# Performance work log

Measured on AMD Instinct MI355X. Metric: run time of the kernel, lower is better.

## Reference

```python
import jax, jax.numpy as jnp
import numpy as np

B, S, D, H = 4, 1024, 1024, 16
DH = D // H  # 64
SCALE = 1.0 / np.sqrt(D)  # module uses 1/sqrt(d_model), not d_head


def _mh(t):
    # [B,S,D] -> [B*H,S,DH]
    b, s, _ = t.shape
    return t.reshape(b, s, H, DH).transpose(0, 2, 1, 3).reshape(b * H, s, DH)


def _shift(t):
    # pad one zero at FRONT of last dim, reinterpret (row-major) as [BH,L+1,S], drop first row
    bh, s, l = t.shape
    t = jnp.concatenate([jnp.zeros((bh, s, 1), t.dtype), t], axis=-1)
    return t.reshape(bh, l + 1, s)[:, 1:, :]


def setup_inputs() -> dict:
    key = jax.random.key(0)
    ks = jax.random.split(key, 12)
    w_sc = 1.0 / np.sqrt(D)
    return {
        "x": jax.random.normal(ks[0], (B, S, D), jnp.float32),
        "u": jax.random.normal(ks[1], (DH,), jnp.float32) * 0.02,
        "v": jax.random.normal(ks[2], (DH,), jnp.float32) * 0.02,
        "pos": jax.random.normal(ks[3], (B, S, D), jnp.float32),
        "Wq": jax.random.normal(ks[4], (D, D), jnp.float32) * w_sc,
        "bq": jnp.zeros((D,), jnp.float32),
        "Wk": jax.random.normal(ks[5], (D, D), jnp.float32) * w_sc,
        "bk": jnp.zeros((D,), jnp.float32),
        "Wv": jax.random.normal(ks[6], (D, D), jnp.float32) * w_sc,
        "bv": jnp.zeros((D,), jnp.float32),
        "Wc": jax.random.normal(ks[7], (D, D), jnp.float32) * w_sc,
        "bc": jnp.zeros((D,), jnp.float32),
    }


def reference(x, u, v, pos, Wq, bq, Wk, bk, Wv, bv, Wc, bc):
    q = _mh(x @ Wq.T + bq)      # [BH,S,DH]
    k = _mh(x @ Wk.T + bk)      # [BH,S,DH]
    w = _mh(x @ Wv.T + bv)      # [BH,S,DH]
    r = _mh(pos)                # [BH,S,DH]
    ac = jnp.einsum('bjk,bmk->bjm', q + u, k)          # content-content  [BH,S,S]
    bd = _shift(jnp.einsum('bjk,blk->bjl', q + v, r))  # content-position [BH,S,S]
    att = jax.nn.softmax((ac + bd) * SCALE, axis=-1)   # dropout is identity (eval)
    o = att @ w                                        # [BH,S,DH]
    o = o.reshape(B, H, S, DH).transpose(0, 2, 1, 3).reshape(B, S, D)
    return o @ Wc.T + bc
```

## Files before the change

kernel.cpp:

```cpp
#include <hip/hip_runtime.h>
#include <hip/hip_bf16.h>


typedef __bf16 bf16x8 __attribute__((ext_vector_type(8)));
typedef float  f32x4  __attribute__((ext_vector_type(4)));
typedef unsigned short u16x4 __attribute__((ext_vector_type(4)));

struct alignas(16) U128 { unsigned long long lo, hi; };

__device__ __forceinline__ bf16x8 ldg8(const __hip_bfloat16* p) {
    U128 u = *reinterpret_cast<const U128*>(p);
    return __builtin_bit_cast(bf16x8, u);
}

__device__ __forceinline__ __bf16 f2b(float f) {
    __hip_bfloat16 h = __float2bfloat16(f);
    return __builtin_bit_cast(__bf16, h);
}
__device__ __forceinline__ unsigned short f2bu(float f) {
    __hip_bfloat16 h = __float2bfloat16(f);
    return __builtin_bit_cast(unsigned short, h);
}
__device__ __forceinline__ float b2f(__bf16 b) {
    __hip_bfloat16 h = __builtin_bit_cast(__hip_bfloat16, b);
    return __bfloat162float(h);
}
__device__ __forceinline__ float bu2f(unsigned short u) {
    __hip_bfloat16 h = __builtin_bit_cast(__hip_bfloat16, u);
    return __bfloat162float(h);
}

__device__ __forceinline__ bf16x8 ldg8cvt(const float* p) {
    f32x4 a = *reinterpret_cast<const f32x4*>(p);
    f32x4 b = *reinterpret_cast<const f32x4*>(p + 4);
    bf16x8 r;
    r[0] = f2b(a[0]); r[1] = f2b(a[1]); r[2] = f2b(a[2]); r[3] = f2b(a[3]);
    r[4] = f2b(b[0]); r[5] = f2b(b[1]); r[6] = f2b(b[2]); r[7] = f2b(b[3]);
    return r;
}

#define MFMA16(a, b, c) __builtin_amdgcn_mfma_f32_16x16x32_bf16((a), (b), (c), 0, 0, 0)

__device__ __forceinline__ void gll16(const __hip_bfloat16* g, void* lds_wave_base) {
    __builtin_amdgcn_global_load_lds(
        (const __attribute__((address_space(1))) void*)g,
        (__attribute__((address_space(3))) void*)lds_wave_base,
        16, 0, 0);
}

__global__ __launch_bounds__(256) void cvt_kernel(
    const float* __restrict__ x,  const float* __restrict__ pos,
    const float* __restrict__ wq, const float* __restrict__ wk,
    const float* __restrict__ wv, const float* __restrict__ wc,
    __hip_bfloat16* __restrict__ xb, __hip_bfloat16* __restrict__ posb,
    __hip_bfloat16* __restrict__ wqkvb, __hip_bfloat16* __restrict__ wcb)
{
    const size_t base = ((size_t)blockIdx.x * 256 + threadIdx.x) * 8;
    const size_t M1 = (size_t)1 << 20;
    const float* src; __hip_bfloat16* dst; size_t o;
    if (base < 4*M1)        { src = x;   dst = xb;           o = base; }
    else if (base < 8*M1)   { src = pos; dst = posb;         o = base - 4*M1; }
    else if (base < 9*M1)   { src = wq;  dst = wqkvb;        o = base - 8*M1; }
    else if (base < 10*M1)  { src = wk;  dst = wqkvb + M1;   o = base - 9*M1; }
    else if (base < 11*M1)  { src = wv;  dst = wqkvb + 2*M1; o = base - 10*M1; }
    else                    { src = wc;  dst = wcb;          o = base - 11*M1; }
    *(bf16x8*)(dst + o) = ldg8cvt(src + o);
}

__global__ __launch_bounds__(256) void gemm_qkv(
    const __hip_bfloat16* __restrict__ A,
    const __hip_bfloat16* __restrict__ Bm,
    const float* __restrict__ bq, const float* __restrict__ bk,
    const float* __restrict__ bv, const float* __restrict__ u,
    __hip_bfloat16* __restrict__ Qu,
    __hip_bfloat16* __restrict__ Kb, __hip_bfloat16* __restrict__ Vt)
{
    __shared__ __hip_bfloat16 As[128 * 32];
    __shared__ __hip_bfloat16 Bs[128 * 32];

    const int tid  = threadIdx.x;
    const int lane = tid & 63, w = tid >> 6;
    const int quad = lane >> 4, c16 = lane & 15;
    const int wm = w >> 1, wn = w & 1;
    const int m0 = blockIdx.y * 128;
    const int n0 = blockIdx.x * 128;

    const int srow = w * 16 + (lane >> 2);
    const int scol = (lane & 3) * 8;
    const __hip_bfloat16* gA0 = A  + (size_t)(m0 + srow) * 1024 + scol;
    const __hip_bfloat16* gA1 = gA0 + (size_t)64 * 1024;
    const __hip_bfloat16* gB0 = Bm + (size_t)(n0 + srow) * 1024 + scol;
    const __hip_bfloat16* gB1 = gB0 + (size_t)64 * 1024;
    char* ldsA0 = (char*)As + (w << 10);
    char* ldsA1 = ldsA0 + 4096;
    char* ldsB0 = (char*)Bs + (w << 10);
    char* ldsB1 = ldsB0 + 4096;

    f32x4 acc[4][4] = {};

    for (int k0 = 0; k0 < 1024; k0 += 32) {
        gll16(gA0 + k0, ldsA0);
        gll16(gA1 + k0, ldsA1);
        gll16(gB0 + k0, ldsB0);
        gll16(gB1 + k0, ldsB1);
        __syncthreads();

        bf16x8 af[4], bfr[4];
        #pragma unroll
        for (int i = 0; i < 4; ++i) {
            af[i]  = *(const bf16x8*)&As[(wm * 64 + i * 16 + c16) * 32 + quad * 8];
            bfr[i] = *(const bf16x8*)&Bs[(wn * 64 + i * 16 + c16) * 32 + quad * 8];
        }
        #pragma unroll
        for (int mi = 0; mi < 4; ++mi)
            #pragma unroll
            for (int ni = 0; ni < 4; ++ni)
                acc[mi][ni] = MFMA16(af[mi], bfr[ni], acc[mi][ni]);
        __syncthreads();
    }

    #pragma unroll
    for (int mi = 0; mi < 4; ++mi) {
        #pragma unroll
        for (int ni = 0; ni < 4; ++ni) {
            const int m = m0 + wm * 64 + mi * 16 + quad * 4;
            const int n = n0 + wn * 64 + ni * 16 + c16;
            if (n < 1024) {
                const float b0 = bq[n] + u[n & 63];
                #pragma unroll
                for (int r = 0; r < 4; ++r)
                    Qu[(size_t)(m + r) * 1024 + n] =
                        __float2bfloat16(acc[mi][ni][r] + b0);
            } else if (n < 2048) {
                const int nn = n - 1024;
                const float b0 = bk[nn];
                #pragma unroll
                for (int r = 0; r < 4; ++r)
                    Kb[(size_t)(m + r) * 1024 + nn] =
                        __float2bfloat16(acc[mi][ni][r] + b0);
            } else {
                const int nn = n - 2048;
                const float b0 = bv[nn];
                const int d = nn & 63, hh = nn >> 6;
                const int bb = m >> 10, s = m & 1023;
                u16x4 pk;
                #pragma unroll
                for (int r = 0; r < 4; ++r)
                    pk[r] = f2bu(acc[mi][ni][r] + b0);
                *(u16x4*)&Vt[(((size_t)(bb * 16 + hh) * 64 + d) << 10) + s] = pk;
            }
        }
    }
}

__global__ __launch_bounds__(256) void gemm_fin64(
    const __hip_bfloat16* __restrict__ A,
    const __hip_bfloat16* __restrict__ Bm,
    float* __restrict__ dout, const float* __restrict__ bc)
{
    __shared__ __hip_bfloat16 As[64 * 32];
    __shared__ __hip_bfloat16 Bs[64 * 32];

    const int tid  = threadIdx.x;
    const int lane = tid & 63, w = tid >> 6;
    const int quad = lane >> 4, c16 = lane & 15;
    const int wm = w >> 1, wn = w & 1;
    const int m0 = blockIdx.y * 64;
    const int n0 = blockIdx.x * 64;

    const int srow = w * 16 + (lane >> 2);
    const int scol = (lane & 3) * 8;
    const __hip_bfloat16* gA = A  + (size_t)(m0 + srow) * 1024 + scol;
    const __hip_bfloat16* gB = Bm + (size_t)(n0 + srow) * 1024 + scol;
    char* ldsA = (char*)As + (w << 10);
    char* ldsB = (char*)Bs + (w << 10);

    f32x4 acc[2][2] = {};

    for (int k0 = 0; k0 < 1024; k0 += 32) {
        gll16(gA + k0, ldsA);
        gll16(gB + k0, ldsB);
        __syncthreads();

        bf16x8 af[2], bfr[2];
        #pragma unroll
        for (int i = 0; i < 2; ++i) {
            af[i]  = *(const bf16x8*)&As[(wm * 32 + i * 16 + c16) * 32 + quad * 8];
            bfr[i] = *(const bf16x8*)&Bs[(wn * 32 + i * 16 + c16) * 32 + quad * 8];
        }
        #pragma unroll
        for (int mi = 0; mi < 2; ++mi)
            #pragma unroll
            for (int ni = 0; ni < 2; ++ni)
                acc[mi][ni] = MFMA16(af[mi], bfr[ni], acc[mi][ni]);
        __syncthreads();
    }

    #pragma unroll
    for (int mi = 0; mi < 2; ++mi) {
        #pragma unroll
        for (int ni = 0; ni < 2; ++ni) {
            const int m = m0 + wm * 32 + mi * 16 + quad * 4;
            const int n = n0 + wn * 32 + ni * 16 + c16;
            const float b0 = bc[n];
            #pragma unroll
            for (int r = 0; r < 4; ++r)
                dout[(size_t)(m + r) * 1024 + n] = acc[mi][ni][r] + b0;
        }
    }
}

__device__ __forceinline__ int lidx16(int row, int c) {
    return (row << 10) + ((((c >> 3) ^ row) << 3) | (c & 7));
}

__global__ __launch_bounds__(512, 4) void attn_kernel(
    const __hip_bfloat16* __restrict__ Qu,
    const __hip_bfloat16* __restrict__ Kb,
    const __hip_bfloat16* __restrict__ Posb,
    const __hip_bfloat16* __restrict__ Vt,
    const float* __restrict__ uvec, const float* __restrict__ vvec,
    __hip_bfloat16* __restrict__ O)
{
    __shared__ __attribute__((aligned(16))) __hip_bfloat16 Ls[32 * 1024];
    __shared__ float q2s[64];
    __shared__ float Wsum[32 * 8];
    __shared__ float rs[32];

    const int tid  = threadIdx.x;
    const int lane = tid & 63, w = tid >> 6;
    const int quad = lane >> 4, c16 = lane & 15;
    const int i0 = blockIdx.y * 32;
    const int bh = blockIdx.x;
    const int b = bh >> 4, h = bh & 15;
    const size_t headoff = (size_t)h * 64;
    const size_t tokbase = (size_t)b * 1024;
    const int j2 = i0 + 32;

    if (tid < 64) {
        float val = 0.f;
        if (j2 < 1024)
            val = b2f(__builtin_bit_cast(__bf16,
                      Qu[(tokbase + j2) * 1024 + headoff + tid])) +
                  (vvec[tid] - uvec[tid]);
        q2s[tid] = val;
    }
    __syncthreads();

    if (tid < 32) {
        const int i = i0 + tid;
        if (i + 1 < 1024) Ls[lidx16(tid, i + 1)] = __float2bfloat16(0.f);
    }

    const __hip_bfloat16* qup0 =
        Qu + (tokbase + i0 + c16) * 1024 + headoff + quad * 8;

    {
        bf16x8 a[2][2];
        #pragma unroll
        for (int g = 0; g < 2; ++g) {
            a[g][0] = ldg8(qup0 + (size_t)g * 16 * 1024);
            a[g][1] = ldg8(qup0 + (size_t)g * 16 * 1024 + 32);
            #pragma unroll
            for (int j = 0; j < 8; ++j) {
                const int d = quad * 8 + j;
                a[g][0][j] = f2b(b2f(a[g][0][j]) + (vvec[d] - uvec[d]));
                a[g][1][j] = f2b(b2f(a[g][1][j]) + (vvec[d + 32] - uvec[d + 32]));
            }
        }
        for (int t = 0; t < 8; ++t) {
            const int l0 = w * 128 + t * 16;
            const __hip_bfloat16* rp =
                Posb + (tokbase + l0 + c16) * 1024 + headoff + quad * 8;
            const bf16x8 r0 = ldg8(rp);
            const bf16x8 r1 = ldg8(rp + 32);
            const int lq = l0 + quad * 4;
            #pragma unroll
            for (int g = 0; g < 2; ++g) {
                f32x4 c = (f32x4){0.f, 0.f, 0.f, 0.f};
                c = MFMA16(r0, a[g][0], c);
                c = MFMA16(r1, a[g][1], c);
                const int jl = g * 16 + c16;
                const int base2 = lq + i0 + jl + 1;
                const int rwm1 = jl - 1;
                #pragma unroll
                for (int r = 0; r < 4; ++r) {
                    const int t1 = base2 + r;
                    const int cc = t1 & 1023;
                    const int rw = rwm1 + (t1 >> 10);
                    if (rw >= 0)
                        Ls[lidx16(rw, cc)] = __float2bfloat16(c[r]);
                }
            }
        }
    }

    if (j2 < 1024) {
        for (int c = i0 + 33 + tid; c < 1024; c += 512) {
            const int l = c - i0 - 33;
            const __hip_bfloat16* rp = Posb + (tokbase + l) * 1024 + headoff;
            float s = 0.f;
            #pragma unroll
            for (int d8 = 0; d8 < 8; ++d8) {
                const bf16x8 rv = ldg8(rp + d8 * 8);
                #pragma unroll
                for (int jj = 0; jj < 8; ++jj)
                    s += q2s[d8 * 8 + jj] * b2f(rv[jj]);
            }
            Ls[lidx16(31, c)] = __float2bfloat16(s);
        }
    }
    __syncthreads();

    {
        bf16x8 au[2][2];
        #pragma unroll
        for (int g = 0; g < 2; ++g) {
            au[g][0] = ldg8(qup0 + (size_t)g * 16 * 1024);
            au[g][1] = ldg8(qup0 + (size_t)g * 16 * 1024 + 32);
        }
        const float C1 = 1.44269504f * 0.03125f;
        const float C2 = -5.77078016f;
        float rsum[2] = {0.f, 0.f};
        for (int t = 0; t < 8; ++t) {
            const int c0 = w * 128 + t * 16;
            const __hip_bfloat16* kp =
                Kb + (tokbase + c0 + c16) * 1024 + headoff + quad * 8;
            const bf16x8 k0 = ldg8(kp);
            const bf16x8 k1 = ldg8(kp + 32);
            const int cc0 = c0 + quad * 4;
            #pragma unroll
            for (int g = 0; g < 2; ++g) {
                f32x4 c = (f32x4){0.f, 0.f, 0.f, 0.f};
                c = MFMA16(k0, au[g][0], c);
                c = MFMA16(k1, au[g][1], c);
                const int jl = g * 16 + c16;
                const int idx = lidx16(jl, cc0);
                const u16x4 bd = *(const u16x4*)&Ls[idx];
                u16x4 pk;
                float s4 = 0.f;
                #pragma unroll
                for (int r = 0; r < 4; ++r) {
                    const float lg = bu2f(bd[r]) + c[r];
                    const float p = __builtin_amdgcn_exp2f(fmaf(lg, C1, C2));
                    s4 += p;
                    pk[r] = f2bu(p);
                }
                *(u16x4*)&Ls[idx] = pk;
                s4 += __shfl_xor(s4, 16);
                s4 += __shfl_xor(s4, 32);
                rsum[g] += s4;
            }
        }
        if (lane < 16) {
            Wsum[lane * 8 + w] = rsum[0];
            Wsum[(16 + lane) * 8 + w] = rsum[1];
        }
    }
    __syncthreads();

    if (tid < 32) {
        float s = 0.f;
        #pragma unroll
        for (int k = 0; k < 8; ++k) s += Wsum[tid * 8 + k];
        rs[tid] = 1.f / s;
    }
    __syncthreads();

    {
        const int d0 = (w & 3) * 16;
        const int kh = w >> 2;
        const __hip_bfloat16* vp =
            Vt + ((size_t)bh * 64 + d0 + c16) * 1024 + quad * 8;
        f32x4 acc[2] = {};
        for (int kk = kh * 512; kk < kh * 512 + 512; kk += 32) {
            const bf16x8 vld = ldg8(vp + kk);
            #pragma unroll
            for (int g = 0; g < 2; ++g) {
                const bf16x8 p =
                    *(const bf16x8*)&Ls[lidx16(g * 16 + c16, kk + quad * 8)];
                acc[g] = MFMA16(p, vld, acc[g]);
            }
        }
        __syncthreads();
        float* Lf = (float*)Ls;
        const int sbase = (w & 3) * 1024;
        if (kh == 1) {
            #pragma unroll
            for (int g = 0; g < 2; ++g)
                #pragma unroll
                for (int r = 0; r < 4; ++r)
                    Lf[sbase + g * 256 + (quad * 4 + r) * 16 + c16] = acc[g][r];
        }
        __syncthreads();
        if (kh == 0) {
            #pragma unroll
            for (int g = 0; g < 2; ++g)
                #pragma unroll
                for (int r = 0; r < 4; ++r) {
                    const int il = g * 16 + quad * 4 + r;
                    const float val =
                        (acc[g][r] + Lf[sbase + g * 256 + (quad * 4 + r) * 16 + c16])
                        * rs[il];
                    const int i = i0 + il;
                    const int d = d0 + c16;
                    O[(tokbase + i) * 1024 + headoff + d] = __float2bfloat16(val);
                }
        }
    }
}

extern "C" void kernel_launch(void* const* d_in, const int* in_sizes, int n_in,
                              void* d_out, int out_size, void* d_ws, size_t ws_size,
                              hipStream_t stream)
{
    const float* x   = (const float*)d_in[0];
    const float* u   = (const float*)d_in[1];
    const float* v   = (const float*)d_in[2];
    const float* pos = (const float*)d_in[3];
    const float* Wq  = (const float*)d_in[4];
    const float* bq  = (const float*)d_in[5];
    const float* Wk  = (const float*)d_in[6];
    const float* bk  = (const float*)d_in[7];
    const float* Wv  = (const float*)d_in[8];
    const float* bv  = (const float*)d_in[9];
    const float* Wc  = (const float*)d_in[10];
    const float* bc  = (const float*)d_in[11];

    const size_t MB = (size_t)1 << 20;
    char* ws = (char*)d_ws;
    __hip_bfloat16* Qu    = (__hip_bfloat16*)(ws + 0 * MB);
    __hip_bfloat16* Kb    = (__hip_bfloat16*)(ws + 8 * MB);
    __hip_bfloat16* Vt    = (__hip_bfloat16*)(ws + 16 * MB);
    __hip_bfloat16* xb    = (__hip_bfloat16*)(ws + 24 * MB);
    __hip_bfloat16* O     = (__hip_bfloat16*)(ws + 24 * MB);
    __hip_bfloat16* Posb  = (__hip_bfloat16*)(ws + 32 * MB);
    __hip_bfloat16* Wqkvb = (__hip_bfloat16*)(ws + 40 * MB);
    __hip_bfloat16* Wcb   = (__hip_bfloat16*)(ws + 46 * MB);

    cvt_kernel<<<6144, 256, 0, stream>>>(x, pos, Wq, Wk, Wv, Wc,
                                         xb, Posb, Wqkvb, Wcb);

    gemm_qkv<<<dim3(24, 32), dim3(256), 0, stream>>>(
        xb, Wqkvb, bq, bk, bv, u, Qu, Kb, Vt);

    attn_kernel<<<dim3(64, 32), dim3(512), 0, stream>>>(
        Qu, Kb, Posb, Vt, u, v, O);

    gemm_fin64<<<dim3(16, 64), dim3(256), 0, stream>>>(
        O, Wcb, (float*)d_out, bc);
}
```

Before: 289.6 us.

## Double attention row tile to 64 and enlarge output GEMM tiles to 128x128

```diff
diff --git a/kernel.cpp b/kernel.cpp
--- a/kernel.cpp
+++ b/kernel.cpp
@@ -153,55 +153,61 @@
     }
 }
 
-__global__ __launch_bounds__(256) void gemm_fin64(
+__global__ __launch_bounds__(256) void gemm_fin(
     const __hip_bfloat16* __restrict__ A,
     const __hip_bfloat16* __restrict__ Bm,
     float* __restrict__ dout, const float* __restrict__ bc)
 {
-    __shared__ __hip_bfloat16 As[64 * 32];
-    __shared__ __hip_bfloat16 Bs[64 * 32];
+    __shared__ __hip_bfloat16 As[128 * 32];
+    __shared__ __hip_bfloat16 Bs[128 * 32];
 
     const int tid  = threadIdx.x;
     const int lane = tid & 63, w = tid >> 6;
     const int quad = lane >> 4, c16 = lane & 15;
     const int wm = w >> 1, wn = w & 1;
-    const int m0 = blockIdx.y * 64;
-    const int n0 = blockIdx.x * 64;
+    const int m0 = blockIdx.y * 128;
+    const int n0 = blockIdx.x * 128;
 
     const int srow = w * 16 + (lane >> 2);
     const int scol = (lane & 3) * 8;
-    const __hip_bfloat16* gA = A  + (size_t)(m0 + srow) * 1024 + scol;
-    const __hip_bfloat16* gB = Bm + (size_t)(n0 + srow) * 1024 + scol;
-    char* ldsA = (char*)As + (w << 10);
-    char* ldsB = (char*)Bs + (w << 10);
-
-    f32x4 acc[2][2] = {};
+    const __hip_bfloat16* gA0 = A  + (size_t)(m0 + srow) * 1024 + scol;
+    const __hip_bfloat16* gA1 = gA0 + (size_t)64 * 1024;
+    const __hip_bfloat16* gB0 = Bm + (size_t)(n0 + srow) * 1024 + scol;
+    const __hip_bfloat16* gB1 = gB0 + (size_t)64 * 1024;
+    char* ldsA0 = (char*)As + (w << 10);
+    char* ldsA1 = ldsA0 + 4096;
+    char* ldsB0 = (char*)Bs + (w << 10);
+    char* ldsB1 = ldsB0 + 4096;
+
+    f32x4 acc[4][4] = {};
 
     for (int k0 = 0; k0 < 1024; k0 += 32) {
-        gll16(gA + k0, ldsA);
-        gll16(gB + k0, ldsB);
-        __syncthreads();
-
-        bf16x8 af[2], bfr[2];
-        #pragma unroll
-        for (int i = 0; i < 2; ++i) {
-            af[i]  = *(const bf16x8*)&As[(wm * 32 + i * 16 + c16) * 32 + quad * 8];
-            bfr[i] = *(const bf16x8*)&Bs[(wn * 32 + i * 16 + c16) * 32 + quad * 8];
-        }
-        #pragma unroll
-        for (int mi = 0; mi < 2; ++mi)
-            #pragma unroll
-            for (int ni = 0; ni < 2; ++ni)
+        gll16(gA0 + k0, ldsA0);
+        gll16(gA1 + k0, ldsA1);
+        gll16(gB0 + k0, ldsB0);
+        gll16(gB1 + k0, ldsB1);
+        __syncthreads();
+
+        bf16x8 af[4], bfr[4];
+        #pragma unroll
+        for (int i = 0; i < 4; ++i) {
+            af[i]  = *(const bf16x8*)&As[(wm * 64 + i * 16 + c16) * 32 + quad * 8];
+            bfr[i] = *(const bf16x8*)&Bs[(wn * 64 + i * 16 + c16) * 32 + quad * 8];
+        }
+        #pragma unroll
+        for (int mi = 0; mi < 4; ++mi)
+            #pragma unroll
+            for (int ni = 0; ni < 4; ++ni)
                 acc[mi][ni] = MFMA16(af[mi], bfr[ni], acc[mi][ni]);
         __syncthreads();
     }
 
     #pragma unroll
-    for (int mi = 0; mi < 2; ++mi) {
-        #pragma unroll
-        for (int ni = 0; ni < 2; ++ni) {
-            const int m = m0 + wm * 32 + mi * 16 + quad * 4;
-            const int n = n0 + wn * 32 + ni * 16 + c16;
+    for (int mi = 0; mi < 4; ++mi) {
+        #pragma unroll
+        for (int ni = 0; ni < 4; ++ni) {
+            const int m = m0 + wm * 64 + mi * 16 + quad * 4;
+            const int n = n0 + wn * 64 + ni * 16 + c16;
             const float b0 = bc[n];
             #pragma unroll
             for (int r = 0; r < 4; ++r)
@@ -214,7 +220,7 @@
     return (row << 10) + ((((c >> 3) ^ row) << 3) | (c & 7));
 }
 
-__global__ __launch_bounds__(512, 4) void attn_kernel(
+__global__ __launch_bounds__(512, 2) void attn_kernel(
     const __hip_bfloat16* __restrict__ Qu,
     const __hip_bfloat16* __restrict__ Kb,
     const __hip_bfloat16* __restrict__ Posb,
@@ -222,32 +228,22 @@
     const float* __restrict__ uvec, const float* __restrict__ vvec,
     __hip_bfloat16* __restrict__ O)
 {
-    __shared__ __attribute__((aligned(16))) __hip_bfloat16 Ls[32 * 1024];
-    __shared__ float q2s[64];
-    __shared__ float Wsum[32 * 8];
-    __shared__ float rs[32];
+    __shared__ __attribute__((aligned(16))) __hip_bfloat16 Ls[64 * 1024];
+    __shared__ float Wsum[64 * 8];
+    __shared__ float rs[64];
 
     const int tid  = threadIdx.x;
     const int lane = tid & 63, w = tid >> 6;
     const int quad = lane >> 4, c16 = lane & 15;
-    const int i0 = blockIdx.y * 32;
+    const int i0 = blockIdx.y * 64;
     const int bh = blockIdx.x;
     const int b = bh >> 4, h = bh & 15;
     const size_t headoff = (size_t)h * 64;
     const size_t tokbase = (size_t)b * 1024;
-    const int j2 = i0 + 32;
+    const int j2 = i0 + 64;
+    const bool havej2 = (j2 < 1024);
 
     if (tid < 64) {
-        float val = 0.f;
-        if (j2 < 1024)
-            val = b2f(__builtin_bit_cast(__bf16,
-                      Qu[(tokbase + j2) * 1024 + headoff + tid])) +
-                  (vvec[tid] - uvec[tid]);
-        q2s[tid] = val;
-    }
-    __syncthreads();
-
-    if (tid < 32) {
         const int i = i0 + tid;
         if (i + 1 < 1024) Ls[lidx16(tid, i + 1)] = __float2bfloat16(0.f);
     }
@@ -256,9 +252,9 @@
         Qu + (tokbase + i0 + c16) * 1024 + headoff + quad * 8;
 
     {
-        bf16x8 a[2][2];
-        #pragma unroll
-        for (int g = 0; g < 2; ++g) {
+        bf16x8 a[4][2];
+        #pragma unroll
+        for (int g = 0; g < 4; ++g) {
             a[g][0] = ldg8(qup0 + (size_t)g * 16 * 1024);
             a[g][1] = ldg8(qup0 + (size_t)g * 16 * 1024 + 32);
             #pragma unroll
@@ -266,6 +262,17 @@
                 const int d = quad * 8 + j;
                 a[g][0][j] = f2b(b2f(a[g][0][j]) + (vvec[d] - uvec[d]));
                 a[g][1][j] = f2b(b2f(a[g][1][j]) + (vvec[d + 32] - uvec[d + 32]));
+            }
+        }
+        bf16x8 a4[2];
+        if (havej2) {
+            a4[0] = ldg8(qup0 + (size_t)64 * 1024);
+            a4[1] = ldg8(qup0 + (size_t)64 * 1024 + 32);
+            #pragma unroll
+            for (int j = 0; j < 8; ++j) {
+                const int d = quad * 8 + j;
+                a4[0][j] = f2b(b2f(a4[0][j]) + (vvec[d] - uvec[d]));
+                a4[1][j] = f2b(b2f(a4[1][j]) + (vvec[d + 32] - uvec[d + 32]));
             }
         }
         for (int t = 0; t < 8; ++t) {
@@ -276,7 +283,7 @@
             const bf16x8 r1 = ldg8(rp + 32);
             const int lq = l0 + quad * 4;
             #pragma unroll
-            for (int g = 0; g < 2; ++g) {
+            for (int g = 0; g < 4; ++g) {
                 f32x4 c = (f32x4){0.f, 0.f, 0.f, 0.f};
                 c = MFMA16(r0, a[g][0], c);
                 c = MFMA16(r1, a[g][1], c);
@@ -292,36 +299,33 @@
                         Ls[lidx16(rw, cc)] = __float2bfloat16(c[r]);
                 }
             }
-        }
-    }
-
-    if (j2 < 1024) {
-        for (int c = i0 + 33 + tid; c < 1024; c += 512) {
-            const int l = c - i0 - 33;
-            const __hip_bfloat16* rp = Posb + (tokbase + l) * 1024 + headoff;
-            float s = 0.f;
-            #pragma unroll
-            for (int d8 = 0; d8 < 8; ++d8) {
-                const bf16x8 rv = ldg8(rp + d8 * 8);
-                #pragma unroll
-                for (int jj = 0; jj < 8; ++jj)
-                    s += q2s[d8 * 8 + jj] * b2f(rv[jj]);
-            }
-            Ls[lidx16(31, c)] = __float2bfloat16(s);
+            if (havej2) {
+                f32x4 c = (f32x4){0.f, 0.f, 0.f, 0.f};
+                c = MFMA16(r0, a4[0], c);
+                c = MFMA16(r1, a4[1], c);
+                if (c16 == 0) {
+                    #pragma unroll
+                    for (int r = 0; r < 4; ++r) {
+                        const int cc = lq + r + i0 + 65;
+                        if (cc < 1024)
+                            Ls[lidx16(63, cc)] = __float2bfloat16(c[r]);
+                    }
+                }
+            }
         }
     }
     __syncthreads();
 
     {
-        bf16x8 au[2][2];
-        #pragma unroll
-        for (int g = 0; g < 2; ++g) {
+        bf16x8 au[4][2];
+        #pragma unroll
+        for (int g = 0; g < 4; ++g) {
             au[g][0] = ldg8(qup0 + (size_t)g * 16 * 1024);
             au[g][1] = ldg8(qup0 + (size_t)g * 16 * 1024 + 32);
         }
         const float C1 = 1.44269504f * 0.03125f;
         const float C2 = -5.77078016f;
-        float rsum[2] = {0.f, 0.f};
+        float rsum[4] = {0.f, 0.f, 0.f, 0.f};
         for (int t = 0; t < 8; ++t) {
             const int c0 = w * 128 + t * 16;
             const __hip_bfloat16* kp =
@@ -330,7 +334,7 @@
             const bf16x8 k1 = ldg8(kp + 32);
             const int cc0 = c0 + quad * 4;
             #pragma unroll
-            for (int g = 0; g < 2; ++g) {
+            for (int g = 0; g < 4; ++g) {
                 f32x4 c = (f32x4){0.f, 0.f, 0.f, 0.f};
                 c = MFMA16(k0, au[g][0], c);
                 c = MFMA16(k1, au[g][1], c);
@@ -353,13 +357,14 @@
             }
         }
         if (lane < 16) {
-            Wsum[lane * 8 + w] = rsum[0];
-            Wsum[(16 + lane) * 8 + w] = rsum[1];
+            #pragma unroll
+            for (int g = 0; g < 4; ++g)
+                Wsum[(g * 16 + lane) * 8 + w] = rsum[g];
         }
     }
     __syncthreads();
 
-    if (tid < 32) {
+    if (tid < 64) {
         float s = 0.f;
         #pragma unroll
         for (int k = 0; k < 8; ++k) s += Wsum[tid * 8 + k];
@@ -372,11 +377,11 @@
         const int kh = w >> 2;
         const __hip_bfloat16* vp =
             Vt + ((size_t)bh * 64 + d0 + c16) * 1024 + quad * 8;
-        f32x4 acc[2] = {};
+        f32x4 acc[4] = {};
         for (int kk = kh * 512; kk < kh * 512 + 512; kk += 32) {
             const bf16x8 vld = ldg8(vp + kk);
             #pragma unroll
-            for (int g = 0; g < 2; ++g) {
+            for (int g = 0; g < 4; ++g) {
                 const bf16x8 p =
                     *(const bf16x8*)&Ls[lidx16(g * 16 + c16, kk + quad * 8)];
                 acc[g] = MFMA16(p, vld, acc[g]);
@@ -387,7 +392,7 @@
         const int sbase = (w & 3) * 1024;
         if (kh == 1) {
             #pragma unroll
-            for (int g = 0; g < 2; ++g)
+            for (int g = 0; g < 4; ++g)
                 #pragma unroll
                 for (int r = 0; r < 4; ++r)
                     Lf[sbase + g * 256 + (quad * 4 + r) * 16 + c16] = acc[g][r];
@@ -395,7 +400,7 @@
         __syncthreads();
         if (kh == 0) {
             #pragma unroll
-            for (int g = 0; g < 2; ++g)
+            for (int g = 0; g < 4; ++g)
                 #pragma unroll
                 for (int r = 0; r < 4; ++r) {
                     const int il = g * 16 + quad * 4 + r;
@@ -444,9 +449,9 @@
     gemm_qkv<<<dim3(24, 32), dim3(256), 0, stream>>>(
         xb, Wqkvb, bq, bk, bv, u, Qu, Kb, Vt);
 
-    attn_kernel<<<dim3(64, 32), dim3(512), 0, stream>>>(
+    attn_kernel<<<dim3(64, 16), dim3(512), 0, stream>>>(
         Qu, Kb, Posb, Vt, u, v, O);
 
-    gemm_fin64<<<dim3(16, 64), dim3(256), 0, stream>>>(
+    gemm_fin<<<dim3(8, 32), dim3(256), 0, stream>>>(
         O, Wcb, (float*)d_out, bc);
 }
```

Measured after the change: 266.6 us. 1.09x faster.
